# Kernel tuning notes

Measured on AMD Instinct MI355X. Metric: run time of the kernel, lower is better.

The kernel has to match this reference:

```python
import jax, jax.numpy as jnp
import numpy as np

N = 1024
HID, STEM_CH = 256, 64
BN_OUT, ST_OUT, MLP = 128, 64, 256
MORPH, BN_WS, ST_WS = 31, 11, 31
FH = FW = 256
VH = VW = 1024
VIS_PS, FUSED_PS = 0.1, 0.4
DELTA_SCALE, EPS = 1.5, 1e-8


def _gauss(ws):
    y = np.linspace(-1.0, 1.0, ws)
    yy, xx = np.meshgrid(y, y, indexing='ij')
    g = np.exp(-(xx ** 2 + yy ** 2) / (2 * 0.4 ** 2))
    return jnp.asarray((g / g.sum())[None, None], dtype=jnp.float32)

BN_GAUSS = _gauss(BN_WS)
ST_GAUSS = _gauss(ST_WS)


def _gelu(x):
    return jax.nn.gelu(x, approximate=False)


def _softplus_inverse(x, eps=1e-6):
    x = jnp.maximum(x, eps)
    return x + jnp.log(-jnp.expm1(-x))


def _normalise(t, eps=EPS):
    t = jnp.maximum(t, 0.0)
    return t / (t.sum(axis=(-2, -1), keepdims=True) + eps)


def _extract_windows(fmap, pos, ws):
    # fmap: [1,C,H,W]; pos: [N,2] = (x,y) float pixel coords -> [N,C,ws,ws] via bilinear gather
    f = fmap[0]
    C, H, W = f.shape
    half = ws // 2
    offs = jnp.arange(ws, dtype=pos.dtype) - half
    xs = jnp.clip(pos[:, 0:1] + offs, 0.0, W - 1.0)  # [N,ws]
    ys = jnp.clip(pos[:, 1:2] + offs, 0.0, H - 1.0)
    x0 = jnp.clip(jnp.floor(xs), 0, W - 2).astype(jnp.int32)
    y0 = jnp.clip(jnp.floor(ys), 0, H - 2).astype(jnp.int32)
    wx = (xs - x0)[:, None, :]   # [N,1,ws]
    wy = (ys - y0)[:, :, None]   # [N,ws,1]
    X0, Y0 = x0[:, None, :], y0[:, :, None]
    v00 = f[:, Y0, X0]
    v01 = f[:, Y0, X0 + 1]
    v10 = f[:, Y0 + 1, X0]
    v11 = f[:, Y0 + 1, X0 + 1]   # each [C,N,ws,ws]
    out = (v00 * (1 - wy) * (1 - wx) + v01 * (1 - wy) * wx
           + v10 * wy * (1 - wx) + v11 * wy * wx)
    return out.transpose(1, 0, 2, 3)


def _convnext_block(x, dw_w, dw_b, ln_g, ln_b, pw1_w, pw1_b, pw2_w, pw2_b, gamma):
    C = x.shape[1]
    h = jax.lax.conv_general_dilated(x, dw_w, (1, 1), [(3, 3), (3, 3)],
        dimension_numbers=('NCHW', 'OIHW', 'NCHW'), feature_group_count=C)
    h = h + dw_b[None, :, None, None]
    h = h.transpose(0, 2, 3, 1)  # NHWC
    mu = h.mean(-1, keepdims=True)
    var = ((h - mu) ** 2).mean(-1, keepdims=True)
    h = (h - mu) / jnp.sqrt(var + 1e-6) * ln_g + ln_b
    h = _gelu(h @ pw1_w.T + pw1_b)
    h = (h @ pw2_w.T + pw2_b) * gamma
    return x + h.transpose(0, 3, 1, 2)


def _conv3x3(x, w, b):
    return jax.lax.conv_general_dilated(x, w, (1, 1), [(1, 1), (1, 1)],
        dimension_numbers=('NCHW', 'OIHW', 'NCHW')) + b[None, :, None, None]


def setup_inputs() -> dict:
    key = jax.random.key(0)
    ks = jax.random.split(key, 24)

    def w(i, shape, fan_in):
        return jax.random.normal(ks[i], shape, jnp.float32) / np.sqrt(fan_in)

    inp = {}
    inp['bottleneck'] = jax.random.normal(ks[0], (1, HID, FH, FW), jnp.float32)
    inp['vis_stem_features'] = jax.random.normal(ks[1], (1, STEM_CH, VH, VW), jnp.float32)
    inp['source_positions_vis'] = 20.0 + jax.random.uniform(ks[2], (N, 2), jnp.float32) * 980.0
    inp['init_morphology'] = jax.random.uniform(ks[3], (N, MORPH, MORPH), jnp.float32) + 1e-3
    # ConvNeXt block params
    inp['dw_w'] = w(4, (HID, 1, 7, 7), 49)
    inp['dw_b'] = jnp.zeros((HID,), jnp.float32)
    inp['ln_g'] = jnp.ones((HID,), jnp.float32)
    inp['ln_b'] = jnp.zeros((HID,), jnp.float32)
    inp['pw1_w'] = w(5, (4 * HID, HID), HID)
    inp['pw1_b'] = jnp.zeros((4 * HID,), jnp.float32)
    inp['pw2_w'] = w(6, (HID, 4 * HID), 4 * HID)
    inp['pw2_b'] = jnp.zeros((HID,), jnp.float32)
    inp['ls_gamma'] = 0.1 * jnp.ones((HID,), jnp.float32)
    # bottleneck 1x1 projection
    inp['bn_w'] = w(7, (BN_OUT, HID, 1, 1), HID)
    inp['bn_b'] = jnp.zeros((BN_OUT,), jnp.float32)
    # stem conv stack
    inp['st1_w'] = w(8, (ST_OUT, STEM_CH, 3, 3), 9 * STEM_CH)
    inp['st1_b'] = jnp.zeros((ST_OUT,), jnp.float32)
    inp['st2_w'] = w(9, (ST_OUT, ST_OUT, 3, 3), 9 * ST_OUT)
    inp['st2_b'] = jnp.zeros((ST_OUT,), jnp.float32)
    # trunk MLP
    feat_dim = BN_OUT + ST_OUT
    inp['tr1_w'] = w(10, (MLP, feat_dim), feat_dim)
    inp['tr1_b'] = jnp.zeros((MLP,), jnp.float32)
    inp['tr2_w'] = w(11, (MLP, MLP), MLP)
    inp['tr2_b'] = jnp.zeros((MLP,), jnp.float32)
    # morph delta head (small instead of exact zeros so the path is exercised)
    inp['md_w'] = 0.01 * w(12, (MORPH * MORPH, MLP), MLP)
    inp['md_b'] = jnp.zeros((MORPH * MORPH,), jnp.float32)
    inp['fused_h'] = FH
    inp['fused_w'] = FW
    inp['vis_h'] = VH
    inp['vis_w'] = VW
    return inp


def reference(bottleneck, vis_stem_features, source_positions_vis, init_morphology,
              dw_w, dw_b, ln_g, ln_b, pw1_w, pw1_b, pw2_w, pw2_b, ls_gamma,
              bn_w, bn_b, st1_w, st1_b, st2_w, st2_b,
              tr1_w, tr1_b, tr2_w, tr2_b, md_w, md_b,
              fused_h, fused_w, vis_h, vis_w):
    init_morph = _normalise(init_morphology)
    # VIS px -> bottleneck px (pixel-center-aligned affine between resolutions)
    s = VIS_PS / FUSED_PS
    pos_bn = (source_positions_vis + 0.5) * s - 0.5
    # bottleneck branch
    bn_win = _extract_windows(bottleneck, pos_bn, BN_WS)  # [N,HID,11,11]
    h = _convnext_block(bn_win, dw_w, dw_b, ln_g, ln_b, pw1_w, pw1_b, pw2_w, pw2_b, ls_gamma)
    h = _gelu(jnp.einsum('nchw,oc->nohw', h, bn_w[:, :, 0, 0]) + bn_b[None, :, None, None])
    bn_vec = (h * BN_GAUSS).sum(axis=(-2, -1))  # [N,BN_OUT]
    # stem branch
    st_win = _extract_windows(vis_stem_features, source_positions_vis, ST_WS)  # [N,64,31,31]
    g = _gelu(_conv3x3(st_win, st1_w, st1_b))
    g = _gelu(_conv3x3(g, st2_w, st2_b))
    st_vec = (g * ST_GAUSS).sum(axis=(-2, -1))  # [N,ST_OUT]
    feat = jnp.concatenate([bn_vec, st_vec], axis=1)
    hid = _gelu(feat @ tr1_w.T + tr1_b)
    hid = _gelu(hid @ tr2_w.T + tr2_b)
    delta = jnp.tanh(hid @ md_w.T + md_b).reshape(init_morph.shape)
    base_logits = _softplus_inverse(jnp.maximum(init_morph, EPS), eps=EPS)
    morphology = _normalise(jax.nn.softplus(base_logits + DELTA_SCALE * delta))
    return morphology, delta, feat
```

## Files before the change

### kernel.cpp

```cpp
#include <hip/hip_runtime.h>
#include <math.h>

#define N_SRC 1024
#define VHW 1024
#define FHW 256
#define MQ 30976

typedef __attribute__((ext_vector_type(8))) short short8;
typedef __attribute__((ext_vector_type(4))) float f32x4;

#define MFMA_B16(a,b,c) __builtin_amdgcn_mfma_f32_16x16x32_bf16((a),(b),(c),0,0,0)

__device__ __forceinline__ float gelu_f(float x){
  return 0.5f * x * (1.0f + erff(x * 0.70710678118654752440f));
}
__device__ __forceinline__ unsigned short f2bf(float f){
  union { float f; unsigned u; } x; x.f = f;
  unsigned r = x.u + 0x7fffu + ((x.u >> 16) & 1u);
  return (unsigned short)(r >> 16);
}
__device__ __forceinline__ float bf2f(unsigned short h){
  union { unsigned u; float f; } x; x.u = ((unsigned)h) << 16;
  return x.f;
}

__global__ void k_gauss(float* __restrict__ gbn, float* __restrict__ gst){
  __shared__ double red[256];
  int t = threadIdx.x;
  {
    double v = 0.0;
    if (t < 121){
      int r = t / 11, c = t % 11;
      double y = -1.0 + 2.0 * (double)r / 10.0;
      double x = -1.0 + 2.0 * (double)c / 10.0;
      v = exp(-(x*x + y*y) / (2.0 * 0.4 * 0.4));
    }
    red[t] = v; __syncthreads();
    for (int s = 128; s > 0; s >>= 1){ if (t < s) red[t] += red[t+s]; __syncthreads(); }
    double sum = red[0];
    __syncthreads();
    if (t < 121) gbn[t] = (float)(v / sum);
    __syncthreads();
  }
  {
    double vals[4]; double loc = 0.0;
    #pragma unroll
    for (int i = 0; i < 4; ++i){
      int j = t + 256*i;
      double v = 0.0;
      if (j < 961){
        int r = j / 31, c = j % 31;
        double y = -1.0 + 2.0 * (double)r / 30.0;
        double x = -1.0 + 2.0 * (double)c / 30.0;
        v = exp(-(x*x + y*y) / (2.0 * 0.4 * 0.4));
      }
      vals[i] = v; loc += v;
    }
    red[t] = loc; __syncthreads();
    for (int s = 128; s > 0; s >>= 1){ if (t < s) red[t] += red[t+s]; __syncthreads(); }
    double sum = red[0];
    __syncthreads();
    #pragma unroll
    for (int i = 0; i < 4; ++i){
      int j = t + 256*i;
      if (j < 961) gst[j] = (float)(vals[i] / sum);
    }
  }
}

__global__ void k_trans(const float* __restrict__ pw1_w, const float* __restrict__ pw2_w,
                        const float* __restrict__ bn_w,
                        const float* __restrict__ st1_w, const float* __restrict__ st2_w,
                        unsigned short* __restrict__ W1b, unsigned short* __restrict__ W2b,
                        unsigned short* __restrict__ bnWb,
                        unsigned short* __restrict__ Wc1, unsigned short* __restrict__ Wc2){
  int stride = gridDim.x * blockDim.x;
  int i0 = blockIdx.x * blockDim.x + threadIdx.x;
  for (int e = i0; e < 256*1024; e += stride) W1b[e] = f2bf(pw1_w[e]);
  for (int e = i0; e < 256*1024; e += stride) W2b[e] = f2bf(pw2_w[e]);
  for (int e = i0; e < 128*256; e += stride) bnWb[e] = f2bf(bn_w[e]);
  for (int e = i0; e < 64*576; e += stride){
    int co = e / 576, r = e % 576, d = r >> 6, ci = r & 63;
    Wc1[e] = f2bf(st1_w[(co*64 + ci)*9 + d]);
    Wc2[e] = f2bf(st2_w[(co*64 + ci)*9 + d]);
  }
}


__global__ __launch_bounds__(256) void k_stg(
    const float* __restrict__ vis, const float* __restrict__ pos,
    unsigned short* __restrict__ v_win)
{
  int b = blockIdx.x;
  int n = b >> 1, h = b & 1;
  float px = pos[2*n], py = pos[2*n + 1];
  int e0 = h * 3844;
  for (int e = e0 + threadIdx.x; e < e0 + 3844; e += 256){
    int cg = e / 961, p = e - cg*961;
    int r = p / 31, c = p - r*31;
    float xsf = fminf(fmaxf(px + (float)(c - 15), 0.f), 1023.f);
    float ysf = fminf(fmaxf(py + (float)(r - 15), 0.f), 1023.f);
    int x0 = min((int)xsf, 1022);
    int y0 = min((int)ysf, 1022);
    float wx = xsf - (float)x0, wy = ysf - (float)y0;
    float w00 = (1.f-wy)*(1.f-wx), w01 = (1.f-wy)*wx;
    float w10 = wy*(1.f-wx),       w11 = wy*wx;
    size_t off = (size_t)y0*VHW + x0;
    const float* bp = vis + (size_t)(cg*8)*(VHW*VHW) + off;
    short8 v;
    #pragma unroll
    for (int i = 0; i < 8; ++i){
      const float* bb = bp + (size_t)i*(VHW*VHW);
      v[i] = (short)f2bf(bb[0]*w00 + bb[1]*w01 + bb[VHW]*w10 + bb[VHW+1]*w11);
    }
    *(short8*)&v_win[((size_t)cg*(1024*961) + (size_t)n*961 + p)*8] = v;
  }
}

template<int NP>
__device__ __forceinline__ void conv_tiles_g1(
    const unsigned short* __restrict__ in_t, const short8* B0,
    int pb0, int pb1, int lk, f32x4& a00, f32x4& a10)
{
  const unsigned short* a0p = in_t + (lk*NP + pb0)*8;
  const unsigned short* a1p = in_t + (lk*NP + pb1)*8;
  #pragma unroll
  for (int ks = 0; ks < 18; ++ks){
    const int d = ks >> 1;
    const int dy = d / 3, dx = d - dy*3;
    const int off = (((ks & 1) ? 4*NP : 0) + dy*33 + dx) * 8;
    short8 A0 = *(const short8*)&a0p[off];
    short8 A1 = *(const short8*)&a1p[off];
    a00 = MFMA_B16(A0, B0[ks], a00);
    a10 = MFMA_B16(A1, B0[ks], a10);
  }
}

#define BANDR 6
#define NPA 330
#define NPB 264

__global__ __launch_bounds__(512, 4) void k_stconv(
    const unsigned short* __restrict__ v_win,
    const unsigned short* __restrict__ Wc1, const float* __restrict__ st1_b,
    const unsigned short* __restrict__ Wc2, const float* __restrict__ st2_b,
    const float* __restrict__ gst, float* __restrict__ st_vec)
{
  __shared__ __align__(16) unsigned short As[NPA*64];
  __shared__ __align__(16) unsigned short Bs[NPB*64];
  int n = blockIdx.x, band = blockIdx.y;
  int t = threadIdx.x;
  int w = t >> 6, l = t & 63, lr = l & 15, lk = l >> 4;
  int co0 = (w & 3) * 16;
  int mh = w >> 2;
  int ybaseV = band*BANDR - 2;
  int ybaseG = band*BANDR - 1;
  int rows_out = min(BANDR, 31 - band*BANDR);

  #pragma unroll
  for (int cg = 0; cg < 8; ++cg){
    for (int p = t; p < NPA; p += 512){
      int gr = p / 33, gc = p - gr*33;
      int yy = ybaseV + gr, xx = gc - 1;
      short8 v = {0,0,0,0,0,0,0,0};
      if (yy >= 0 && yy < 31 && xx >= 0 && xx < 31)
        v = *(const short8*)&v_win[((size_t)cg*(1024*961) + (size_t)n*961 + yy*31 + xx)*8];
      *(short8*)&As[(cg*NPA + p)*8] = v;
    }
  }
  {
    short8 z = {0,0,0,0,0,0,0,0};
    for (int c = t; c < NPB*8; c += 512)
      *(short8*)&Bs[c*8] = z;
  }
  __syncthreads();

  {
    short8 B0[18];
    #pragma unroll
    for (int ks = 0; ks < 18; ++ks)
      B0[ks] = *(const short8*)&Wc1[(co0 + lr)*576 + ks*32 + lk*8];
    const int npos1 = 8*31;
    const int ntiles1 = 16;
    int mstart = mh * 8;
    int mend = min(mstart + 8, ntiles1);
    float bc0 = st1_b[co0 + lr];
    int c0 = co0 + lr;

    for (int mt = mstart; mt < mend; mt += 2){
      int s0 = min(mt*16 + lr, npos1 - 1);
      int s1 = min(mt*16 + 16 + lr, npos1 - 1);
      int ly0 = s0 / 31, x0p = s0 - ly0*31;
      int ly1 = s1 / 31, x1p = s1 - ly1*31;
      int pb0 = ly0*33 + x0p, pb1 = ly1*33 + x1p;
      f32x4 a00 = {0,0,0,0}, a10 = {0,0,0,0};
      conv_tiles_g1<NPA>(As, B0, pb0, pb1, lk, a00, a10);
      #pragma unroll
      for (int i = 0; i < 4; ++i){
        int spo = mt*16 + lk*4 + i;
        if (spo < npos1){
          int ly = spo / 31, xx = spo - ly*31;
          int yy1 = ybaseG + ly;
          if (yy1 >= 0 && yy1 <= 30){
            int pB = ly*33 + xx + 1;
            Bs[((c0 >> 3)*NPB + pB)*8 + (c0 & 7)] = f2bf(gelu_f(a00[i] + bc0));
          }
        }
        int sp1 = spo + 16;
        if (sp1 < npos1 && mt + 1 < mend){
          int ly = sp1 / 31, xx = sp1 - ly*31;
          int yy1 = ybaseG + ly;
          if (yy1 >= 0 && yy1 <= 30){
            int pB = ly*33 + xx + 1;
            Bs[((c0 >> 3)*NPB + pB)*8 + (c0 & 7)] = f2bf(gelu_f(a10[i] + bc0));
          }
        }
      }
    }
  }
  __syncthreads();

  {
    short8 B0[18];
    #pragma unroll
    for (int ks = 0; ks < 18; ++ks)
      B0[ks] = *(const short8*)&Wc2[(co0 + lr)*576 + ks*32 + lk*8];
    int npos = rows_out * 31;
    int ntiles = (npos + 15) >> 4;
    int per = (ntiles + 1) >> 1;
    int mstart = mh * per;
    int mend = min(mstart + per, ntiles);
    float bc0 = st2_b[co0 + lr];
    float vacc0 = 0.f;

    for (int mt = mstart; mt < mend; mt += 2){
      int s0 = min(mt*16 + lr, npos - 1);
      int s1 = min(mt*16 + 16 + lr, npos - 1);
      int ly0 = s0 / 31, x0p = s0 - ly0*31;
      int ly1 = s1 / 31, x1p = s1 - ly1*31;
      int pb0 = ly0*33 + x0p, pb1 = ly1*33 + x1p;
      f32x4 a00 = {0,0,0,0}, a10 = {0,0,0,0};
      conv_tiles_g1<NPB>(Bs, B0, pb0, pb1, lk, a00, a10);
      #pragma unroll
      for (int i = 0; i < 4; ++i){
        int spo = mt*16 + lk*4 + i;
        if (spo < npos){
          int ly = spo / 31, xx = spo - ly*31;
          float wt = gst[(band*BANDR + ly)*31 + xx];
          vacc0 += wt * gelu_f(a00[i] + bc0);
        }
        int sp1 = spo + 16;
        if (sp1 < npos && mt + 1 < mend){
          int ly = sp1 / 31, xx = sp1 - ly*31;
          float wt = gst[(band*BANDR + ly)*31 + xx];
          vacc0 += wt * gelu_f(a10[i] + bc0);
        }
      }
    }
    vacc0 += __shfl_xor(vacc0, 16); vacc0 += __shfl_xor(vacc0, 32);
    if (lk == 0)
      atomicAdd(&st_vec[n*64 + co0 + lr], vacc0);
  }
}

__global__ __launch_bounds__(512, 4) void k_bnpre(
  const float* __restrict__ bott, const float* __restrict__ pos,
  const float* __restrict__ dw_w, const float* __restrict__ dw_b,
  unsigned short* __restrict__ x_bf, unsigned short* __restrict__ dcob)
{
  __shared__ float xt[128*123];
  __shared__ float wt4[121*4];
  __shared__ int   wo[121];
  int n = blockIdx.x, ch0 = blockIdx.y * 128;
  int t = threadIdx.x;
  float pbx = (pos[2*n]   + 0.5f)*0.25f - 0.5f;
  float pby = (pos[2*n+1] + 0.5f)*0.25f - 0.5f;

  if (t < 121){
    int r = t / 11, c = t - r*11;
    float xsf = fminf(fmaxf(pbx + (float)(c-5), 0.f), 255.f);
    float ysf = fminf(fmaxf(pby + (float)(r-5), 0.f), 255.f);
    int x0 = min((int)xsf, 254);
    int y0 = min((int)ysf, 254);
    float wx = xsf - (float)x0, wy = ysf - (float)y0;
    wo[t] = y0*FHW + x0;
    wt4[t*4+0] = (1.f-wy)*(1.f-wx);
    wt4[t*4+1] = (1.f-wy)*wx;
    wt4[t*4+2] = wy*(1.f-wx);
    wt4[t*4+3] = wy*wx;
  }
  __syncthreads();

  for (int e = t; e < 128*121; e += 512){
    int ch = e / 121, p = e - ch*121;
    const float* b = bott + (size_t)(ch0 + ch)*(FHW*FHW) + wo[p];
    float4 w = *(const float4*)&wt4[p*4];
    xt[ch*123 + p] = b[0]*w.x + b[1]*w.y + b[FHW]*w.z + b[FHW+1]*w.w;
  }
  __syncthreads();

  for (int e = t; e < 121*64; e += 512){
    int row = e >> 6, cp = (e & 63) << 1;
    float v0 = xt[cp*123 + row], v1 = xt[(cp+1)*123 + row];
    unsigned pk = (unsigned)f2bf(v0) | ((unsigned)f2bf(v1) << 16);
    *(unsigned*)&x_bf[(((size_t)n*121 + row) << 8) + ch0 + cp] = pk;
  }

  int ch = t & 127, part = t >> 7;
  float w[49];
  #pragma unroll
  for (int k = 0; k < 49; ++k) w[k] = dw_w[(ch0 + ch)*49 + k];
  float bias = dw_b[ch0 + ch];
  const float* xc = &xt[ch*123];
  for (int sp = part; sp < 121; sp += 4){
    int r = sp / 11, c = sp - r*11;
    float a = bias;
    #pragma unroll
    for (int dy = 0; dy < 7; ++dy){
      int ry = r + dy - 3;
      bool okr = (ry >= 0) && (ry < 11);
      #pragma unroll
      for (int dx = 0; dx < 7; ++dx){
        int cx = c + dx - 3;
        float xv = (okr && cx >= 0 && cx < 11) ? xc[ry*11 + cx] : 0.f;
        a = fmaf(xv, w[dy*7 + dx], a);
      }
    }
    dcob[(((size_t)n*121 + sp) << 8) + ch0 + ch] = f2bf(a);
  }
}

__global__ __launch_bounds__(256) void k_ln(
  const unsigned short* __restrict__ dcob, const float* __restrict__ ln_g, const float* __restrict__ ln_b,
  unsigned short* __restrict__ normb)
{
  int m = blockIdx.x*4 + (threadIdx.x >> 6);
  int lane = threadIdx.x & 63;
  ushort4 raw = *(const ushort4*)&dcob[(size_t)m*256 + lane*4];
  float4 v = { bf2f(raw.x), bf2f(raw.y), bf2f(raw.z), bf2f(raw.w) };
  float s  = v.x+v.y+v.z+v.w;
  float ss = v.x*v.x + v.y*v.y + v.z*v.z + v.w*v.w;
  #pragma unroll
  for (int off = 32; off; off >>= 1){ s += __shfl_xor(s, off); ss += __shfl_xor(ss, off); }
  float mu  = s * 0.00390625f;
  float var = ss * 0.00390625f - mu*mu;
  float rstd = 1.0f / sqrtf(var + 1e-6f);
  float4 g = *(const float4*)&ln_g[lane*4];
  float4 b = *(const float4*)&ln_b[lane*4];
  ushort4 o;
  o.x = f2bf((v.x-mu)*rstd*g.x + b.x);
  o.y = f2bf((v.y-mu)*rstd*g.y + b.y);
  o.z = f2bf((v.z-mu)*rstd*g.z + b.z);
  o.w = f2bf((v.w-mu)*rstd*g.w + b.w);
  *(ushort4*)&normb[(size_t)m*256 + lane*4] = o;
}


__global__ __launch_bounds__(256, 3) void k_gemm1(
  const unsigned short* __restrict__ A, const unsigned short* __restrict__ B,
  const float* __restrict__ b1, unsigned short* __restrict__ H)
{
  __shared__ __align__(16) unsigned short sm[16384];
  unsigned short* As = sm;
  unsigned short* Bs = sm + 8192;
  int t = threadIdx.x, lane = t & 63, w = t >> 6;
  int lr = lane & 15, lk = lane >> 4;
  int p = blockIdx.x;
  int L = (p & 7) * 242 + (p >> 3);
  int m0 = (L >> 3) * 128, n0 = (L & 7) * 128;

  f32x4 acc[2][8];
  #pragma unroll
  for (int i = 0; i < 2; ++i)
    #pragma unroll
    for (int j = 0; j < 8; ++j) acc[i][j] = (f32x4){0,0,0,0};

  for (int ks = 0; ks < 4; ++ks){
    if (ks) __syncthreads();
    #pragma unroll
    for (int it = 0; it < 4; ++it){
      int j = t + it*256;
      int r = j >> 3, c = j & 7;
      int k8 = c ^ (r & 7);
      *(short8*)&As[j*8] = *(const short8*)&A[(size_t)(m0 + r)*256 + ks*64 + k8*8];
      *(short8*)&Bs[j*8] = *(const short8*)&B[(size_t)(n0 + r)*256 + ks*64 + k8*8];
    }
    __syncthreads();
    #pragma unroll
    for (int kk = 0; kk < 2; ++kk){
      int k8a = kk*4 + lk;
      short8 af[2];
      #pragma unroll
      for (int i = 0; i < 2; ++i){
        int ra = w*32 + i*16 + lr;
        af[i] = *(const short8*)&As[(ra*8 + (k8a ^ (ra & 7)))*8];
      }
      #pragma unroll
      for (int j = 0; j < 8; ++j){
        int rb = j*16 + lr;
        short8 bf = *(const short8*)&Bs[(rb*8 + (k8a ^ (rb & 7)))*8];
        acc[0][j] = MFMA_B16(af[0], bf, acc[0][j]);
        acc[1][j] = MFMA_B16(af[1], bf, acc[1][j]);
      }
    }
  }
  __syncthreads();
  #pragma unroll
  for (int i = 0; i < 2; ++i)
    #pragma unroll
    for (int j = 0; j < 8; ++j){
      int col = j*16 + lr;
      float bb = b1[n0 + col];
      #pragma unroll
      for (int q = 0; q < 4; ++q){
        int row = w*32 + i*16 + lk*4 + q;
        sm[row*128 + col] = f2bf(gelu_f(acc[i][j][q] + bb));
      }
    }
  __syncthreads();
  #pragma unroll
  for (int it = 0; it < 8; ++it){
    int e = t + it*256;
    int row = e >> 4, c8 = e & 15;
    *(short8*)&H[(size_t)(m0 + row)*1024 + n0 + c8*8] = *(const short8*)&sm[row*128 + c8*8];
  }
}

__global__ __launch_bounds__(256, 4) void k_gemm2(
  const unsigned short* __restrict__ A, const unsigned short* __restrict__ B,
  const float* __restrict__ b2v, const float* __restrict__ lsg,
  const unsigned short* __restrict__ xres, unsigned short* __restrict__ Y)
{
  __shared__ __align__(16) unsigned short sm[16384];
  unsigned short* As = sm;
  unsigned short* Bs = sm + 8192;
  int t = threadIdx.x, lane = t & 63, w = t >> 6;
  int lr = lane & 15, lk = lane >> 4;
  int p = blockIdx.x;
  int L = (p & 7) * 121 + (p >> 3);
  int m0 = (L >> 2) * 128, n0 = (L & 3) * 64;

  f32x4 acc[2][4];
  #pragma unroll
  for (int i = 0; i < 2; ++i)
    #pragma unroll
    for (int j = 0; j < 4; ++j) acc[i][j] = (f32x4){0,0,0,0};

  for (int ks = 0; ks < 16; ++ks){
    if (ks) __syncthreads();
    #pragma unroll
    for (int it = 0; it < 4; ++it){
      int j = t + it*256;
      int r = j >> 3, c = j & 7;
      int k8 = c ^ (r & 7);
      *(short8*)&As[j*8] = *(const short8*)&A[(size_t)(m0 + r)*1024 + ks*64 + k8*8];
    }
    #pragma unroll
    for (int it = 0; it < 2; ++it){
      int j = t + it*256;
      int r = j >> 3, c = j & 7;
      int k8 = c ^ (r & 7);
      *(short8*)&Bs[j*8] = *(const short8*)&B[(size_t)(n0 + r)*1024 + ks*64 + k8*8];
    }
    __syncthreads();
    #pragma unroll
    for (int kk = 0; kk < 2; ++kk){
      int k8a = kk*4 + lk;
      short8 af[2];
      #pragma unroll
      for (int i = 0; i < 2; ++i){
        int ra = w*32 + i*16 + lr;
        af[i] = *(const short8*)&As[(ra*8 + (k8a ^ (ra & 7)))*8];
      }
      #pragma unroll
      for (int j = 0; j < 4; ++j){
        int rb = j*16 + lr;
        short8 bf = *(const short8*)&Bs[(rb*8 + (k8a ^ (rb & 7)))*8];
        acc[0][j] = MFMA_B16(af[0], bf, acc[0][j]);
        acc[1][j] = MFMA_B16(af[1], bf, acc[1][j]);
      }
    }
  }
  __syncthreads();
  float* Cs = (float*)sm;
  #pragma unroll
  for (int i = 0; i < 2; ++i)
    #pragma unroll
    for (int j = 0; j < 4; ++j){
      int col = j*16 + lr;
      #pragma unroll
      for (int q = 0; q < 4; ++q){
        int row = w*32 + i*16 + lk*4 + q;
        Cs[row*64 + col] = acc[i][j][q];
      }
    }
  __syncthreads();
  #pragma unroll
  for (int it = 0; it < 8; ++it){
    int e4 = t + it*256;
    int row = e4 >> 4, c4 = (e4 & 15) * 4;
    float4 cv = *(const float4*)&Cs[row*64 + c4];
    size_t grow = (size_t)(m0 + row);
    ushort4 xr = *(const ushort4*)&xres[grow*256 + n0 + c4];
    float4 bb = *(const float4*)&b2v[n0 + c4];
    float4 gm = *(const float4*)&lsg[n0 + c4];
    ushort4 o;
    o.x = f2bf(fmaf(cv.x + bb.x, gm.x, bf2f(xr.x)));
    o.y = f2bf(fmaf(cv.y + bb.y, gm.y, bf2f(xr.y)));
    o.z = f2bf(fmaf(cv.z + bb.z, gm.z, bf2f(xr.z)));
    o.w = f2bf(fmaf(cv.w + bb.w, gm.w, bf2f(xr.w)));
    *(ushort4*)&Y[grow*256 + n0 + c4] = o;
  }
}

__global__ __launch_bounds__(256) void k_bnvec(
  const unsigned short* __restrict__ yb, const unsigned short* __restrict__ bnWb,
  const float* __restrict__ bn_b, const float* __restrict__ gbn, float* __restrict__ bn_vec)
{
  int n = blockIdx.x, t = threadIdx.x;
  int w = t >> 6, l = t & 63, lr = l & 15, lk = l >> 4;
  f32x4 acc[8][2];
  #pragma unroll
  for (int mt = 0; mt < 8; ++mt){ acc[mt][0] = (f32x4){0,0,0,0}; acc[mt][1] = (f32x4){0,0,0,0}; }

  #pragma unroll
  for (int ks = 0; ks < 8; ++ks){
    short8 b0 = *(const short8*)&bnWb[(size_t)(w*32 + lr)*256 + ks*32 + lk*8];
    short8 b1 = *(const short8*)&bnWb[(size_t)(w*32 + 16 + lr)*256 + ks*32 + lk*8];
    #pragma unroll
    for (int mt = 0; mt < 8; ++mt){
      int row = min(mt*16 + lr, 120);
      short8 a = *(const short8*)&yb[((size_t)n*121 + row)*256 + ks*32 + lk*8];
      acc[mt][0] = MFMA_B16(a, b0, acc[mt][0]);
      acc[mt][1] = MFMA_B16(a, b1, acc[mt][1]);
    }
  }

  float s0 = 0.f, s1 = 0.f;
  float bb0 = bn_b[w*32 + lr], bb1 = bn_b[w*32 + 16 + lr];
  #pragma unroll
  for (int mt = 0; mt < 8; ++mt)
    #pragma unroll
    for (int i = 0; i < 4; ++i){
      int row = mt*16 + lk*4 + i;
      if (row < 121){
        float g = gbn[row];
        s0 += g * gelu_f(acc[mt][0][i] + bb0);
        s1 += g * gelu_f(acc[mt][1][i] + bb1);
      }
    }
  s0 += __shfl_xor(s0, 16); s0 += __shfl_xor(s0, 32);
  s1 += __shfl_xor(s1, 16); s1 += __shfl_xor(s1, 32);
  if (lk == 0){
    bn_vec[n*128 + w*32 + lr] = s0;
    bn_vec[n*128 + w*32 + 16 + lr] = s1;
  }
}

__global__ __launch_bounds__(256) void k_head(
  const float* __restrict__ bn_vec, const float* __restrict__ st_vec,
  const float* __restrict__ tr1_w, const float* __restrict__ tr1_b,
  const float* __restrict__ tr2_w, const float* __restrict__ tr2_b,
  const float* __restrict__ md_w, const float* __restrict__ md_b,
  const float* __restrict__ init_m,
  float* __restrict__ out)
{
  __shared__ float feat4[4*192];
  __shared__ float h14[4*256];
  __shared__ float h24[4*256];
  __shared__ float dlt4[4*961];
  __shared__ float yv4[4*961];
  int t = threadIdx.x;
  int n0 = blockIdx.x * 4;
  float* morph_out = out;
  float* delta_out = out + 984064;
  float* feat_out  = out + 1968128;

  for (int e = t; e < 4*192; e += 256){
    int ni = e / 192, j = e - ni*192;
    float v = (j < 128) ? bn_vec[(n0+ni)*128 + j] : st_vec[(n0+ni)*64 + j - 128];
    feat4[e] = v;
    feat_out[(size_t)(n0+ni)*192 + j] = v;
  }
  __syncthreads();
  {
    float a0 = tr1_b[t], a1 = a0, a2 = a0, a3 = a0;
    const float* wr = &tr1_w[t*192];
    for (int k = 0; k < 192; ++k){
      float wk = wr[k];
      a0 = fmaf(feat4[k],       wk, a0);
      a1 = fmaf(feat4[192 + k], wk, a1);
      a2 = fmaf(feat4[384 + k], wk, a2);
      a3 = fmaf(feat4[576 + k], wk, a3);
    }
    h14[t] = gelu_f(a0); h14[256 + t] = gelu_f(a1);
    h14[512 + t] = gelu_f(a2); h14[768 + t] = gelu_f(a3);
  }
  __syncthreads();
  {
    float a0 = tr2_b[t], a1 = a0, a2 = a0, a3 = a0;
    const float* wr = &tr2_w[t*256];
    for (int k = 0; k < 256; ++k){
      float wk = wr[k];
      a0 = fmaf(h14[k],       wk, a0);
      a1 = fmaf(h14[256 + k], wk, a1);
      a2 = fmaf(h14[512 + k], wk, a2);
      a3 = fmaf(h14[768 + k], wk, a3);
    }
    h24[t] = gelu_f(a0); h24[256 + t] = gelu_f(a1);
    h24[512 + t] = gelu_f(a2); h24[768 + t] = gelu_f(a3);
  }
  __syncthreads();
  for (int j = t; j < 961; j += 256){
    float b = md_b[j];
    float a0 = b, a1 = b, a2 = b, a3 = b;
    const float* wr = &md_w[(size_t)j*256];
    for (int k = 0; k < 256; ++k){
      float wk = wr[k];
      a0 = fmaf(h24[k],       wk, a0);
      a1 = fmaf(h24[256 + k], wk, a1);
      a2 = fmaf(h24[512 + k], wk, a2);
      a3 = fmaf(h24[768 + k], wk, a3);
    }
    float d0 = tanhf(a0), d1 = tanhf(a1), d2 = tanhf(a2), d3 = tanhf(a3);
    dlt4[j] = d0; dlt4[961 + j] = d1; dlt4[1922 + j] = d2; dlt4[2883 + j] = d3;
    delta_out[(size_t)(n0+0)*961 + j] = d0;
    delta_out[(size_t)(n0+1)*961 + j] = d1;
    delta_out[(size_t)(n0+2)*961 + j] = d2;
    delta_out[(size_t)(n0+3)*961 + j] = d3;
  }
  __syncthreads();

  int g = t >> 6, l64 = t & 63;
  int n = n0 + g;
  const float* im = &init_m[(size_t)n*961];
  float loc = 0.f;
  for (int j = l64; j < 961; j += 64) loc += fmaxf(im[j], 0.f);
  #pragma unroll
  for (int off = 32; off; off >>= 1) loc += __shfl_xor(loc, off);
  float s0 = loc + 1e-8f;
  float loc2 = 0.f;
  for (int j = l64; j < 961; j += 64){
    float imn = fmaxf(im[j], 0.f) / s0;
    float x = fmaxf(imn, 1e-8f);
    float base = x + logf(-expm1f(-x));
    float z = base + 1.5f * dlt4[g*961 + j];
    float y = fmaxf(z, 0.f) + log1pf(expf(-fabsf(z)));
    yv4[g*961 + j] = y;
    loc2 += y;
  }
  #pragma unroll
  for (int off = 32; off; off >>= 1) loc2 += __shfl_xor(loc2, off);
  float s1 = loc2 + 1e-8f;
  for (int j = l64; j < 961; j += 64)
    morph_out[(size_t)n*961 + j] = yv4[g*961 + j] / s1;
}

extern "C" void kernel_launch(void* const* d_in, const int* in_sizes, int n_in,
                              void* d_out, int out_size, void* d_ws, size_t ws_size,
                              hipStream_t stream)
{
  const float* bott = (const float*)d_in[0];
  const float* vis  = (const float*)d_in[1];
  const float* pos  = (const float*)d_in[2];
  const float* initm= (const float*)d_in[3];
  const float* dw_w = (const float*)d_in[4];
  const float* dw_b = (const float*)d_in[5];
  const float* ln_g = (const float*)d_in[6];
  const float* ln_b = (const float*)d_in[7];
  const float* pw1_w= (const float*)d_in[8];
  const float* pw1_b= (const float*)d_in[9];
  const float* pw2_w= (const float*)d_in[10];
  const float* pw2_b= (const float*)d_in[11];
  const float* lsg  = (const float*)d_in[12];
  const float* bn_w = (const float*)d_in[13];
  const float* bn_b = (const float*)d_in[14];
  const float* st1_w= (const float*)d_in[15];
  const float* st1_b= (const float*)d_in[16];
  const float* st2_w= (const float*)d_in[17];
  const float* st2_b= (const float*)d_in[18];
  const float* tr1_w= (const float*)d_in[19];
  const float* tr1_b= (const float*)d_in[20];
  const float* tr2_w= (const float*)d_in[21];
  const float* tr2_b= (const float*)d_in[22];
  const float* md_w = (const float*)d_in[23];
  const float* md_b = (const float*)d_in[24];

  char* ws = (char*)d_ws;
  unsigned short* v_win = (unsigned short*)(ws);
  unsigned short* dcob  = (unsigned short*)(ws);
  unsigned short* Hq    = (unsigned short*)(ws);
  unsigned short* yb    = (unsigned short*)(ws + 63438848);
  unsigned short* x_bf  = (unsigned short*)(ws + 126877696);
  unsigned short* normb = (unsigned short*)(ws + 190316544);
  char* S = ws + 253755392;
  float* st_vec = (float*)(S);
  float* bn_vec = (float*)(S + 262144);
  float* gbn    = (float*)(S + 786432);
  float* gst    = (float*)(S + 786944);
  unsigned short* W1b  = (unsigned short*)(S + 791040);
  unsigned short* W2b  = (unsigned short*)(S + 1315328);
  unsigned short* Wc1  = (unsigned short*)(S + 1839616);
  unsigned short* Wc2  = (unsigned short*)(S + 1913344);
  unsigned short* bnWb = (unsigned short*)(S + 1987072);

  hipMemsetAsync(st_vec, 0, 1024*64*sizeof(float), stream);
  k_gauss<<<1, 256, 0, stream>>>(gbn, gst);
  k_trans<<<256, 256, 0, stream>>>(pw1_w, pw2_w, bn_w, st1_w, st2_w, W1b, W2b, bnWb, Wc1, Wc2);

  k_stg<<<2048, 256, 0, stream>>>(vis, pos, v_win);
  k_stconv<<<dim3(1024, 6), 512, 0, stream>>>(v_win, Wc1, st1_b, Wc2, st2_b, gst, st_vec);

  k_bnpre<<<dim3(1024, 2), 512, 0, stream>>>(bott, pos, dw_w, dw_b, x_bf, dcob);
  k_ln<<<30976, 256, 0, stream>>>(dcob, ln_g, ln_b, normb);

  for (int q = 0; q < 4; ++q){
    size_t ro = (size_t)q * MQ;
    k_gemm1<<<1936, 256, 0, stream>>>(normb + ro*256, W1b, pw1_b, Hq);
    k_gemm2<<<968, 256, 0, stream>>>(Hq, W2b, pw2_b, lsg, x_bf + ro*256, yb + ro*256);
  }
  k_bnvec<<<1024, 256, 0, stream>>>(yb, bnWb, bn_b, gbn, bn_vec);

  k_head<<<256, 256, 0, stream>>>(bn_vec, st_vec, tr1_w, tr1_b, tr2_w, tr2_b,
                                  md_w, md_b, initm, (float*)d_out);
}
```

Baseline: 1.258 ms.

## Split stem conv into two kernels via global intermediate; halve MLP GEMM chunks

The fused stem convolution kernel is split into two kernels. The first computes conv1+GELU for non-overlapping 8-row bands and writes the bf16 result to a global buffer. The second reads it back with a halo and computes conv2, GELU and the Gaussian reduction. This removes the halo recomputation of conv1 rows that each 6-row band previously did, at the cost of a full global write and read of the intermediate activation. Separately, the ConvNeXt MLP GEMMs now run in 2 larger chunks instead of 4, with the output aliased onto the LayerNorm buffer, which cuts launch count and improves occupancy per launch.

```diff
diff --git a/kernel.cpp b/kernel.cpp
--- a/kernel.cpp
+++ b/kernel.cpp
@@ -4,7 +4,7 @@
 #define N_SRC 1024
 #define VHW 1024
 #define FHW 256
-#define MQ 30976
+#define MQ2 61952
 
 typedef __attribute__((ext_vector_type(8))) short short8;
 typedef __attribute__((ext_vector_type(4))) float f32x4;
@@ -136,87 +136,102 @@
   }
 }
 
-#define BANDR 6
-#define NPA 330
-#define NPB 264
-
-__global__ __launch_bounds__(512, 4) void k_stconv(
+#define SB    8
+#define NPV   330
+#define NPO_S 250
+
+__global__ __launch_bounds__(512, 4) void k_stc1(
     const unsigned short* __restrict__ v_win,
     const unsigned short* __restrict__ Wc1, const float* __restrict__ st1_b,
-    const unsigned short* __restrict__ Wc2, const float* __restrict__ st2_b,
-    const float* __restrict__ gst, float* __restrict__ st_vec)
-{
-  __shared__ __align__(16) unsigned short As[NPA*64];
-  __shared__ __align__(16) unsigned short Bs[NPB*64];
+    unsigned short* __restrict__ g1)
+{
+  __shared__ __align__(16) unsigned short As[NPV*64];
+  __shared__ __align__(16) unsigned short Os[NPO_S*64];
   int n = blockIdx.x, band = blockIdx.y;
   int t = threadIdx.x;
   int w = t >> 6, l = t & 63, lr = l & 15, lk = l >> 4;
   int co0 = (w & 3) * 16;
   int mh = w >> 2;
-  int ybaseV = band*BANDR - 2;
-  int ybaseG = band*BANDR - 1;
-  int rows_out = min(BANDR, 31 - band*BANDR);
-
-  #pragma unroll
-  for (int cg = 0; cg < 8; ++cg){
-    for (int p = t; p < NPA; p += 512){
-      int gr = p / 33, gc = p - gr*33;
-      int yy = ybaseV + gr, xx = gc - 1;
-      short8 v = {0,0,0,0,0,0,0,0};
-      if (yy >= 0 && yy < 31 && xx >= 0 && xx < 31)
-        v = *(const short8*)&v_win[((size_t)cg*(1024*961) + (size_t)n*961 + yy*31 + xx)*8];
-      *(short8*)&As[(cg*NPA + p)*8] = v;
-    }
-  }
-  {
-    short8 z = {0,0,0,0,0,0,0,0};
-    for (int c = t; c < NPB*8; c += 512)
-      *(short8*)&Bs[c*8] = z;
-  }
-  __syncthreads();
-
+  int y0 = band*SB;
+  int rows_out = min(SB, 31 - y0);
+  int ybaseV = y0 - 1;
+
+  for (int idx = t; idx < NPV*8; idx += 512){
+    int cg = idx / NPV, p = idx - cg*NPV;
+    int gr = p / 33, gc = p - gr*33;
+    int yy = ybaseV + gr, xx = gc - 1;
+    short8 v = {0,0,0,0,0,0,0,0};
+    if (yy >= 0 && yy < 31 && xx >= 0 && xx < 31)
+      v = *(const short8*)&v_win[((size_t)cg*(1024*961) + (size_t)n*961 + yy*31 + xx)*8];
+    *(short8*)&As[(cg*NPV + p)*8] = v;
+  }
+  __syncthreads();
+
+  int npos = rows_out * 31;
+  int ntiles = (npos + 15) >> 4;
   {
     short8 B0[18];
     #pragma unroll
     for (int ks = 0; ks < 18; ++ks)
       B0[ks] = *(const short8*)&Wc1[(co0 + lr)*576 + ks*32 + lk*8];
-    const int npos1 = 8*31;
-    const int ntiles1 = 16;
-    int mstart = mh * 8;
-    int mend = min(mstart + 8, ntiles1);
     float bc0 = st1_b[co0 + lr];
     int c0 = co0 + lr;
+    int per = (ntiles + 1) >> 1;
+    int mstart = mh * per;
+    int mend = min(mstart + per, ntiles);
 
     for (int mt = mstart; mt < mend; mt += 2){
-      int s0 = min(mt*16 + lr, npos1 - 1);
-      int s1 = min(mt*16 + 16 + lr, npos1 - 1);
+      int s0 = min(mt*16 + lr, npos - 1);
+      int s1 = min(mt*16 + 16 + lr, npos - 1);
       int ly0 = s0 / 31, x0p = s0 - ly0*31;
       int ly1 = s1 / 31, x1p = s1 - ly1*31;
       int pb0 = ly0*33 + x0p, pb1 = ly1*33 + x1p;
       f32x4 a00 = {0,0,0,0}, a10 = {0,0,0,0};
-      conv_tiles_g1<NPA>(As, B0, pb0, pb1, lk, a00, a10);
+      conv_tiles_g1<NPV>(As, B0, pb0, pb1, lk, a00, a10);
       #pragma unroll
       for (int i = 0; i < 4; ++i){
         int spo = mt*16 + lk*4 + i;
-        if (spo < npos1){
-          int ly = spo / 31, xx = spo - ly*31;
-          int yy1 = ybaseG + ly;
-          if (yy1 >= 0 && yy1 <= 30){
-            int pB = ly*33 + xx + 1;
-            Bs[((c0 >> 3)*NPB + pB)*8 + (c0 & 7)] = f2bf(gelu_f(a00[i] + bc0));
-          }
-        }
+        if (spo < npos)
+          Os[((c0 >> 3)*NPO_S + spo)*8 + (c0 & 7)] = f2bf(gelu_f(a00[i] + bc0));
         int sp1 = spo + 16;
-        if (sp1 < npos1 && mt + 1 < mend){
-          int ly = sp1 / 31, xx = sp1 - ly*31;
-          int yy1 = ybaseG + ly;
-          if (yy1 >= 0 && yy1 <= 30){
-            int pB = ly*33 + xx + 1;
-            Bs[((c0 >> 3)*NPB + pB)*8 + (c0 & 7)] = f2bf(gelu_f(a10[i] + bc0));
-          }
-        }
-      }
-    }
+        if (sp1 < npos && mt + 1 < mend)
+          Os[((c0 >> 3)*NPO_S + sp1)*8 + (c0 & 7)] = f2bf(gelu_f(a10[i] + bc0));
+      }
+    }
+  }
+  __syncthreads();
+
+  size_t gbase = (size_t)n*961 + y0*31;
+  for (int idx = t; idx < npos*8; idx += 512){
+    int cg = idx / npos, po = idx - cg*npos;
+    *(short8*)&g1[((size_t)cg*(1024*961) + gbase + po)*8] =
+        *(const short8*)&Os[(cg*NPO_S + po)*8];
+  }
+}
+
+__global__ __launch_bounds__(512, 4) void k_stc2(
+    const unsigned short* __restrict__ g1, const float* __restrict__ gst,
+    const unsigned short* __restrict__ Wc2, const float* __restrict__ st2_b,
+    float* __restrict__ st_vec)
+{
+  __shared__ __align__(16) unsigned short Bs[NPV*64];
+  int n = blockIdx.x, band = blockIdx.y;
+  int t = threadIdx.x;
+  int w = t >> 6, l = t & 63, lr = l & 15, lk = l >> 4;
+  int co0 = (w & 3) * 16;
+  int mh = w >> 2;
+  int y0 = band*SB;
+  int rows_out = min(SB, 31 - y0);
+  int ybaseG = y0 - 1;
+
+  for (int idx = t; idx < NPV*8; idx += 512){
+    int cg = idx / NPV, p = idx - cg*NPV;
+    int gr = p / 33, gc = p - gr*33;
+    int yy = ybaseG + gr, xx = gc - 1;
+    short8 v = {0,0,0,0,0,0,0,0};
+    if (yy >= 0 && yy < 31 && xx >= 0 && xx < 31)
+      v = *(const short8*)&g1[((size_t)cg*(1024*961) + (size_t)n*961 + yy*31 + xx)*8];
+    *(short8*)&Bs[(cg*NPV + p)*8] = v;
   }
   __syncthreads();
 
@@ -240,19 +255,19 @@
       int ly1 = s1 / 31, x1p = s1 - ly1*31;
       int pb0 = ly0*33 + x0p, pb1 = ly1*33 + x1p;
       f32x4 a00 = {0,0,0,0}, a10 = {0,0,0,0};
-      conv_tiles_g1<NPB>(Bs, B0, pb0, pb1, lk, a00, a10);
+      conv_tiles_g1<NPV>(Bs, B0, pb0, pb1, lk, a00, a10);
       #pragma unroll
       for (int i = 0; i < 4; ++i){
         int spo = mt*16 + lk*4 + i;
         if (spo < npos){
           int ly = spo / 31, xx = spo - ly*31;
-          float wt = gst[(band*BANDR + ly)*31 + xx];
+          float wt = gst[(y0 + ly)*31 + xx];
           vacc0 += wt * gelu_f(a00[i] + bc0);
         }
         int sp1 = spo + 16;
         if (sp1 < npos && mt + 1 < mend){
           int ly = sp1 / 31, xx = sp1 - ly*31;
-          float wt = gst[(band*BANDR + ly)*31 + xx];
+          float wt = gst[(y0 + ly)*31 + xx];
           vacc0 += wt * gelu_f(a10[i] + bc0);
         }
       }
@@ -366,7 +381,7 @@
   int t = threadIdx.x, lane = t & 63, w = t >> 6;
   int lr = lane & 15, lk = lane >> 4;
   int p = blockIdx.x;
-  int L = (p & 7) * 242 + (p >> 3);
+  int L = (p & 7) * 484 + (p >> 3);
   int m0 = (L >> 3) * 128, n0 = (L & 7) * 128;
 
   f32x4 acc[2][8];
@@ -437,7 +452,7 @@
   int t = threadIdx.x, lane = t & 63, w = t >> 6;
   int lr = lane & 15, lk = lane >> 4;
   int p = blockIdx.x;
-  int L = (p & 7) * 121 + (p >> 3);
+  int L = (p & 7) * 242 + (p >> 3);
   int m0 = (L >> 2) * 128, n0 = (L & 3) * 64;
 
   f32x4 acc[2][4];
@@ -690,9 +705,10 @@
   unsigned short* v_win = (unsigned short*)(ws);
   unsigned short* dcob  = (unsigned short*)(ws);
   unsigned short* Hq    = (unsigned short*)(ws);
-  unsigned short* yb    = (unsigned short*)(ws + 63438848);
+  unsigned short* g1    = (unsigned short*)(ws + 126877696);
   unsigned short* x_bf  = (unsigned short*)(ws + 126877696);
   unsigned short* normb = (unsigned short*)(ws + 190316544);
+  unsigned short* yb    = normb;
   char* S = ws + 253755392;
   float* st_vec = (float*)(S);
   float* bn_vec = (float*)(S + 262144);
@@ -709,15 +725,16 @@
   k_trans<<<256, 256, 0, stream>>>(pw1_w, pw2_w, bn_w, st1_w, st2_w, W1b, W2b, bnWb, Wc1, Wc2);
 
   k_stg<<<2048, 256, 0, stream>>>(vis, pos, v_win);
-  k_stconv<<<dim3(1024, 6), 512, 0, stream>>>(v_win, Wc1, st1_b, Wc2, st2_b, gst, st_vec);
+  k_stc1<<<dim3(1024, 4), 512, 0, stream>>>(v_win, Wc1, st1_b, g1);
+  k_stc2<<<dim3(1024, 4), 512, 0, stream>>>(g1, gst, Wc2, st2_b, st_vec);
 
   k_bnpre<<<dim3(1024, 2), 512, 0, stream>>>(bott, pos, dw_w, dw_b, x_bf, dcob);
   k_ln<<<30976, 256, 0, stream>>>(dcob, ln_g, ln_b, normb);
 
-  for (int q = 0; q < 4; ++q){
-    size_t ro = (size_t)q * MQ;
-    k_gemm1<<<1936, 256, 0, stream>>>(normb + ro*256, W1b, pw1_b, Hq);
-    k_gemm2<<<968, 256, 0, stream>>>(Hq, W2b, pw2_b, lsg, x_bf + ro*256, yb + ro*256);
+  for (int q = 0; q < 2; ++q){
+    size_t ro = (size_t)q * MQ2;
+    k_gemm1<<<3872, 256, 0, stream>>>(normb + ro*256, W1b, pw1_b, Hq);
+    k_gemm2<<<1936, 256, 0, stream>>>(Hq, W2b, pw2_b, lsg, x_bf + ro*256, yb + ro*256);
   }
   k_bnvec<<<1024, 256, 0, stream>>>(yb, bnWb, bn_b, gbn, bn_vec);
 
```

Result: faster. 1.142 ms, median of 3 (-9.2%).
